# Performance work log

Measured on AMD Instinct MI355X. Metric: run time of the kernel, lower is better.

## Reference

```python
import math
import jax, jax.numpy as jnp
import numpy as np

# static config (mirrors init_kwargs / input_specs)
B, HRV, WRV, CRV = 2, 32, 1024, 64
CB, HB, WB = 256, 200, 200
D, COUT, HEADS, POINTS = 128, 128, 8, 6
DH = D // HEADS
RMAX = 55.0
XMIN, XMAX, YMIN, YMAX = -50.0, 50.0, -50.0, 50.0


def group_norm(x, gamma, beta, groups, eps=1e-5):
    b, h, w, c = x.shape
    xg = x.reshape(b, h, w, groups, c // groups)
    mean = xg.mean(axis=(1, 2, 4), keepdims=True)
    var = xg.var(axis=(1, 2, 4), keepdims=True)
    xg = (xg - mean) * jax.lax.rsqrt(var + eps)
    return xg.reshape(b, h, w, c) * gamma + beta


def fwd(x_rv, bev, pq_w, pq_b, pv_w, pv_b, po_w, po_b, qs_w1, qs_b1, qs_w2, qs_b2,
        rh_w1, rh_b1, rh_g1, rh_be1, rh_w2, rh_g2, rh_be2, rh_w3, rh_b3,
        so_w, so_b, aw_w, aw_b, vp_w, vp_b, op_w, op_b):
    b = x_rv.shape[0]
    nq = HRV * WRV
    az = jnp.linspace(-math.pi, math.pi, WRV + 1)[:-1]  # [Wrv]
    az = jnp.broadcast_to(az[None, None, :], (b, HRV, WRV))
    coord = jnp.stack([jnp.sin(az), jnp.cos(az), jnp.zeros_like(az)], axis=-1)  # [b,H,W,3]
    Q0 = x_rv @ pq_w + pq_b                                  # 1x1 conv as matmul (NHWC)
    Vmap = bev.transpose(0, 2, 3, 1) @ pv_w + pv_b           # [b,HB,WB,D]
    # range head: 1x1 conv -> GN(8) -> GELU -> 3x3 circular conv -> GN(8) -> GELU -> 1x1 conv
    h = jnp.concatenate([x_rv, coord], axis=-1) @ rh_w1 + rh_b1
    h = jax.nn.gelu(group_norm(h, rh_g1, rh_be1, 8), approximate=False)
    hp = jnp.pad(h, ((0, 0), (1, 1), (1, 1), (0, 0)), mode='wrap')  # circular padding
    h = jax.lax.conv_general_dilated(hp, rh_w2, (1, 1), 'VALID',
                                     dimension_numbers=('NHWC', 'HWIO', 'NHWC'))
    h = jax.nn.gelu(group_norm(h, rh_g2, rh_be2, 8), approximate=False)
    rh = h @ rh_w3 + rh_b3                                   # [b,H,W,2]
    mu = jnp.clip(rh[..., 0], 0.0, RMAX)                     # [b,H,W]
    log_sigma = jnp.clip(rh[..., 1:2], -5.0, 3.0)            # [b,H,W,1]
    sigma = jnp.exp(log_sigma)
    x_mu = mu * jnp.cos(az)
    y_mu = mu * jnp.sin(az)
    rx = jnp.clip((x_mu - XMIN) / (XMAX - XMIN), 0.0, 1.0)
    ry = jnp.clip((y_mu - YMIN) / (YMAX - YMIN), 0.0, 1.0)
    ref = jnp.stack([rx, ry], axis=-1).reshape(b, nq, 2)
    sig_feat = jnp.concatenate([log_sigma, 1.0 / (sigma + 1e-6)], axis=-1)
    q = jnp.concatenate([Q0, sig_feat], axis=-1) @ qs_w1 + qs_b1
    q = jax.nn.gelu(q, approximate=False) @ qs_w2 + qs_b2
    query = q.reshape(b, nq, D)
    # ---- MSDA (num_levels = 1) ----
    value = Vmap.reshape(b, HB * WB, D) @ vp_w + vp_b
    vflat = value.reshape(b, HB * WB, HEADS, DH).transpose(0, 2, 1, 3)  # [b,heads,NV,dh]
    offs = (query @ so_w + so_b).reshape(b, nq, HEADS, POINTS, 2)
    attw = jax.nn.softmax((query @ aw_w + aw_b).reshape(b, nq, HEADS, POINTS), axis=-1)
    norm = jnp.array([WB, HB], dtype=query.dtype)            # offset_normalizer = [W, H]
    loc = ref[:, :, None, None, :] + offs / norm             # [b,nq,heads,P,2] in [0,1]
    loc = loc.transpose(0, 2, 1, 3, 4)                       # [b,heads,nq,P,2]
    attw = attw.transpose(0, 2, 1, 3)                        # [b,heads,nq,P]
    # grid_sample bilinear, zero padding, align_corners=False: pix = loc*size - 0.5
    px = loc[..., 0] * WB - 0.5
    py = loc[..., 1] * HB - 0.5
    x0 = jnp.floor(px).astype(jnp.int32)
    y0 = jnp.floor(py).astype(jnp.int32)
    wx = px - x0
    wy = py - y0

    def gather(xi, yi):
        valid = (xi >= 0) & (xi < WB) & (yi >= 0) & (yi < HB)
        idx = jnp.clip(yi, 0, HB - 1) * WB + jnp.clip(xi, 0, WB - 1)
        g = jnp.take_along_axis(vflat, idx.reshape(b, HEADS, nq * POINTS, 1), axis=2)
        return g.reshape(b, HEADS, nq, POINTS, DH) * valid[..., None]

    sampled = (gather(x0, y0) * ((1 - wx) * (1 - wy))[..., None]
               + gather(x0 + 1, y0) * (wx * (1 - wy))[..., None]
               + gather(x0, y0 + 1) * ((1 - wx) * wy)[..., None]
               + gather(x0 + 1, y0 + 1) * (wx * wy)[..., None])    # [b,heads,nq,P,dh]
    out = (sampled * attw[..., None]).sum(axis=3)                  # [b,heads,nq,dh]
    out = out.transpose(0, 2, 1, 3).reshape(b, nq, D) @ op_w + op_b
    y = out.reshape(b, HRV, WRV, D) @ po_w + po_b                  # proj_o (1x1 conv)
    return y                                                       # [b,Hrv,Wrv,C_out]


def setup_inputs() -> dict:
    key = jax.random.key(0)
    ks = jax.random.split(key, 20)
    def rn(i, shape, s=0.02):
        return s * jax.random.normal(ks[i], shape, jnp.float32)
    z = lambda n: jnp.zeros((n,), jnp.float32)
    o = lambda n: jnp.ones((n,), jnp.float32)
    return dict(
        x_rv=rn(0, (B, HRV, WRV, CRV), 1.0),
        bev=rn(1, (B, CB, HB, WB), 1.0),
        pq_w=rn(2, (CRV, D)), pq_b=z(D),
        pv_w=rn(3, (CB, D)), pv_b=z(D),
        po_w=rn(4, (D, COUT)), po_b=z(COUT),
        qs_w1=rn(5, (D + 2, D)), qs_b1=z(D),
        qs_w2=rn(6, (D, D)), qs_b2=z(D),
        rh_w1=rn(7, (CRV + 3, 128)), rh_b1=z(128),
        rh_g1=o(128), rh_be1=z(128),
        rh_w2=rn(8, (3, 3, 128, 64)),
        rh_g2=o(64), rh_be2=z(64),
        rh_w3=rn(9, (64, 2)), rh_b3=z(2),
        so_w=rn(10, (D, HEADS * POINTS * 2)), so_b=rn(11, (HEADS * POINTS * 2,), 0.5),
        aw_w=rn(12, (D, HEADS * POINTS)), aw_b=z(HEADS * POINTS),
        vp_w=rn(13, (D, D)), vp_b=z(D),
        op_w=rn(14, (D, D)), op_b=z(D),
    )


def reference(x_rv, bev, pq_w, pq_b, pv_w, pv_b, po_w, po_b, qs_w1, qs_b1, qs_w2, qs_b2,
              rh_w1, rh_b1, rh_g1, rh_be1, rh_w2, rh_g2, rh_be2, rh_w3, rh_b3,
              so_w, so_b, aw_w, aw_b, vp_w, vp_b, op_w, op_b):
    return fwd(x_rv, bev, pq_w, pq_b, pv_w, pv_b, po_w, po_b, qs_w1, qs_b1, qs_w2, qs_b2,
               rh_w1, rh_b1, rh_g1, rh_be1, rh_w2, rh_g2, rh_be2, rh_w3, rh_b3,
               so_w, so_b, aw_w, aw_b, vp_w, vp_b, op_w, op_b)
```

## Files before the change

kernel.cpp:

```cpp
#include <hip/hip_runtime.h>
#include <math.h>

#define PI_F 3.14159265358979323846f


typedef __attribute__((ext_vector_type(8))) short bf16x8;
typedef __attribute__((ext_vector_type(4))) float f32x4;

__device__ __forceinline__ float gelu_f(float x) {
    return 0.5f * x * (1.0f + erff(x * 0.70710678118654752440f));
}

__device__ __forceinline__ unsigned short f2bf(float x) {
    unsigned int u = __float_as_uint(x);
    u += 0x7fffu + ((u >> 16) & 1u);
    return (unsigned short)(u >> 16);
}

__device__ __forceinline__ float bf2f(unsigned short h) {
    return __uint_as_float((unsigned int)h << 16);
}

__global__ void prep_weights(const float* __restrict__ pv_w, const float* __restrict__ pv_b,
                             const float* __restrict__ vp_w, const float* __restrict__ vp_b,
                             const float* __restrict__ op_w, const float* __restrict__ op_b,
                             const float* __restrict__ po_w, const float* __restrict__ po_b,
                             const float* __restrict__ pq_w, const float* __restrict__ pq_b,
                             const float* __restrict__ qs_w1, const float* __restrict__ qs_b1,
                             const float* __restrict__ qs_w2, const float* __restrict__ qs_b2,
                             const float* __restrict__ so_w, const float* __restrict__ so_b,
                             const float* __restrict__ aw_w, const float* __restrict__ aw_b,
                             const float* __restrict__ rh_w2,
                             unsigned short* __restrict__ wvh, unsigned short* __restrict__ wvl,
                             float* __restrict__ pvvp_b,
                             float* __restrict__ oppo_w, float* __restrict__ oppo_b,
                             float* __restrict__ pqqs_w, float* __restrict__ pqqs_b,
                             float* __restrict__ qsso_w, float* __restrict__ qsso_b,
                             float* __restrict__ qsaw_w, float* __restrict__ qsaw_b,
                             unsigned short* __restrict__ wtb,
                             float2* __restrict__ azsc) {
    int r = blockIdx.x;
    int d = threadIdx.x;
    if (r < 256) {
        float s = 0.f;
        for (int k = 0; k < 128; ++k) s += pv_w[r * 128 + k] * vp_w[k * 128 + d];
        unsigned short h = f2bf(s);
        int dt = d >> 4, mm = d & 15;
        int kc = r >> 5, qd = (r >> 3) & 3, jj = r & 7;
        size_t off = (((size_t)(dt * 8 + kc) * 64) + qd * 16 + mm) * 8 + jj;
        wvh[off] = h;
        wvl[off] = f2bf(s - bf2f(h));
    } else if (r == 256) {
        float s = vp_b[d];
        for (int k = 0; k < 128; ++k) s += pv_b[k] * vp_w[k * 128 + d];
        pvvp_b[d] = s;
    } else if (r < 385) {
        int rr = r - 257;
        float s = 0.f;
        for (int k = 0; k < 128; ++k) s += op_w[rr * 128 + k] * po_w[k * 128 + d];
        oppo_w[rr * 128 + d] = s;
    } else if (r == 385) {
        float s = po_b[d];
        for (int k = 0; k < 128; ++k) s += op_b[k] * po_w[k * 128 + d];
        oppo_b[d] = s;
    } else if (r < 450) {
        int rr = r - 386;
        float s = 0.f;
        for (int k = 0; k < 128; ++k) s += pq_w[rr * 128 + k] * qs_w1[k * 128 + d];
        pqqs_w[rr * 128 + d] = s;
    } else if (r == 450) {
        float s = qs_b1[d];
        for (int k = 0; k < 128; ++k) s += pq_b[k] * qs_w1[k * 128 + d];
        pqqs_b[d] = s;
    } else if (r < 459) {
        int w = (r - 451) * 128 + d;
        float az = -PI_F + (float)w * (6.283185307179586f / 1024.0f);
        azsc[w] = make_float2(sinf(az), cosf(az));
    } else if (r < 587) {
        int rr = r - 459;
        if (d < 96) {
            float s = 0.f;
            for (int k = 0; k < 128; ++k) s += qs_w2[rr * 128 + k] * so_w[k * 96 + d];
            qsso_w[rr * 96 + d] = s;
        }
    } else if (r == 587) {
        if (d < 96) {
            float s = so_b[d];
            for (int k = 0; k < 128; ++k) s += qs_b2[k] * so_w[k * 96 + d];
            qsso_b[d] = s;
        }
    } else if (r < 716) {
        int rr = r - 588;
        if (d < 48) {
            float s = 0.f;
            for (int k = 0; k < 128; ++k) s += qs_w2[rr * 128 + k] * aw_w[k * 48 + d];
            qsaw_w[rr * 48 + d] = s;
        }
    } else if (r == 716) {
        if (d < 48) {
            float s = aw_b[d];
            for (int k = 0; k < 128; ++k) s += qs_b2[k] * aw_w[k * 48 + d];
            qsaw_b[d] = s;
        }
    } else {
        int idx = (r - 717) * 128 + d;
        int ci = idx & 31;
        int o = (idx >> 5) & 63;
        int cc4i = (idx >> 11) & 3;
        int tap = idx >> 13;
        float w = rh_w2[((size_t)tap * 128 + cc4i * 32 + ci) * 64 + o];
        wtb[idx] = f2bf(w);
    }
}

template <int NT, bool STATS>
__global__ __launch_bounds__(2 * NT) void gemm_v3(
    const float* __restrict__ A, int lda,
    const float* __restrict__ W,
    const float* __restrict__ bias,
    float* __restrict__ C, int K,
    const float2* __restrict__ azsc,
    const float* __restrict__ extra2,
    const float* __restrict__ extra_w,
    int emode, int do_gelu, float* __restrict__ stats1) {
    constexpr int NTH = 2 * NT;
    constexpr int NTO = NT / 8;
    __shared__ float As[32][140];
    __shared__ float Ws[32][NT];
    __shared__ float sred[8][2];
    const int tid = threadIdx.x;
    const int tn = tid % NTO;
    const int tm = tid / NTO;
    const int m0 = blockIdx.x * 128;
    if (STATS && tid < 16) sred[tid >> 1][tid & 1] = 0.f;
    float acc[8][8];
#pragma unroll
    for (int i = 0; i < 8; ++i)
#pragma unroll
        for (int j = 0; j < 8; ++j) acc[i][j] = 0.f;

    for (int k0 = 0; k0 < K; k0 += 32) {
        __syncthreads();
        for (int f = tid; f < 1024; f += NTH) {
            int r = f >> 3, c4 = f & 7;
            float4 v = *(const float4*)(A + (size_t)(m0 + r) * lda + k0 + c4 * 4);
            As[c4 * 4 + 0][r] = v.x;
            As[c4 * 4 + 1][r] = v.y;
            As[c4 * 4 + 2][r] = v.z;
            As[c4 * 4 + 3][r] = v.w;
        }
        for (int f = tid; f < 8 * NT; f += NTH) {
            int kk = f / (NT / 4), n4 = f % (NT / 4);
            *(float4*)&Ws[kk][n4 * 4] = *(const float4*)(W + (size_t)(k0 + kk) * NT + n4 * 4);
        }
        __syncthreads();
#pragma unroll 2
        for (int k = 0; k < 32; ++k) {
            const float4 a0 = *(const float4*)&As[k][tm * 8];
            const float4 a1 = *(const float4*)&As[k][tm * 8 + 4];
            const float4 w0 = *(const float4*)&Ws[k][tn * 8];
            const float4 w1 = *(const float4*)&Ws[k][tn * 8 + 4];
            const float av[8] = {a0.x, a0.y, a0.z, a0.w, a1.x, a1.y, a1.z, a1.w};
            const float wv[8] = {w0.x, w0.y, w0.z, w0.w, w1.x, w1.y, w1.z, w1.w};
#pragma unroll
            for (int i = 0; i < 8; ++i)
#pragma unroll
                for (int j = 0; j < 8; ++j) acc[i][j] += av[i] * wv[j];
        }
    }
    float bv[8], e0w[8], e1w[8];
#pragma unroll
    for (int j = 0; j < 8; ++j) bv[j] = bias[tn * 8 + j];
    if (emode) {
#pragma unroll
        for (int j = 0; j < 8; ++j) {
            e0w[j] = extra_w[tn * 8 + j];
            e1w[j] = extra_w[NT + tn * 8 + j];
        }
    }
    float ts = 0.f, ts2 = 0.f;
#pragma unroll
    for (int i = 0; i < 8; ++i) {
        int m = m0 + tm * 8 + i;
        float e0 = 0.f, e1 = 0.f;
        if (emode == 1) {
            float2 sc = azsc[m & 1023];
            e0 = sc.x; e1 = sc.y;
        } else if (emode == 2) {
            e0 = extra2[2 * (size_t)m];
            e1 = extra2[2 * (size_t)m + 1];
        }
        float o[8];
#pragma unroll
        for (int j = 0; j < 8; ++j) {
            float v = acc[i][j] + bv[j];
            if (emode) v += e0 * e0w[j] + e1 * e1w[j];
            if (do_gelu) v = gelu_f(v);
            if (STATS) { ts += v; ts2 += v * v; }
            o[j] = v;
        }
        *(float4*)(C + (size_t)m * NT + tn * 8) = make_float4(o[0], o[1], o[2], o[3]);
        *(float4*)(C + (size_t)m * NT + tn * 8 + 4) = make_float4(o[4], o[5], o[6], o[7]);
    }
    if (STATS) {
        atomicAdd(&sred[tn >> 1][0], ts);
        atomicAdd(&sred[tn >> 1][1], ts2);
        __syncthreads();
        if (tid < 8) {
            int b = m0 >> 15;
            atomicAdd(&stats1[(b * 8 + tid) * 2 + 0], sred[tid][0]);
            atomicAdd(&stats1[(b * 8 + tid) * 2 + 1], sred[tid][1]);
        }
    }
}

template <int MT, int NT, int NTH>
__global__ __launch_bounds__(NTH) void gemm_rn(
    const float* __restrict__ A, int lda,
    const float* __restrict__ W, int ldw,
    const float* __restrict__ bias,
    float* __restrict__ C, int ldc, int K) {
    static_assert(NTH == (MT / 8) * (NT / 4), "thread count mismatch");
    __shared__ float As[32][MT + 12];
    __shared__ float Ws[32][NT];
    constexpr int NTN = NT / 4;
    const int tid = threadIdx.x;
    const int tn = tid % NTN;
    const int tm = tid / NTN;
    const int m0 = blockIdx.x * MT;
    float acc[8][4];
#pragma unroll
    for (int i = 0; i < 8; ++i)
#pragma unroll
        for (int j = 0; j < 4; ++j) acc[i][j] = 0.f;

    for (int k0 = 0; k0 < K; k0 += 32) {
        __syncthreads();
        for (int f = tid; f < MT * 8; f += NTH) {
            int r = f >> 3, c4 = f & 7;
            float4 v = *(const float4*)(A + (size_t)(m0 + r) * lda + k0 + c4 * 4);
            As[c4 * 4 + 0][r] = v.x;
            As[c4 * 4 + 1][r] = v.y;
            As[c4 * 4 + 2][r] = v.z;
            As[c4 * 4 + 3][r] = v.w;
        }
        for (int f = tid; f < 8 * NT; f += NTH) {
            int kk = f / NTN, n4 = f % NTN;
            *(float4*)&Ws[kk][n4 * 4] = *(const float4*)(W + (size_t)(k0 + kk) * ldw + n4 * 4);
        }
        __syncthreads();
#pragma unroll 4
        for (int k = 0; k < 32; ++k) {
            const float4 a0 = *(const float4*)&As[k][tm * 8];
            const float4 a1 = *(const float4*)&As[k][tm * 8 + 4];
            const float4 wv = *(const float4*)&Ws[k][tn * 4];
            acc[0][0] += a0.x * wv.x; acc[0][1] += a0.x * wv.y; acc[0][2] += a0.x * wv.z; acc[0][3] += a0.x * wv.w;
            acc[1][0] += a0.y * wv.x; acc[1][1] += a0.y * wv.y; acc[1][2] += a0.y * wv.z; acc[1][3] += a0.y * wv.w;
            acc[2][0] += a0.z * wv.x; acc[2][1] += a0.z * wv.y; acc[2][2] += a0.z * wv.z; acc[2][3] += a0.z * wv.w;
            acc[3][0] += a0.w * wv.x; acc[3][1] += a0.w * wv.y; acc[3][2] += a0.w * wv.z; acc[3][3] += a0.w * wv.w;
            acc[4][0] += a1.x * wv.x; acc[4][1] += a1.x * wv.y; acc[4][2] += a1.x * wv.z; acc[4][3] += a1.x * wv.w;
            acc[5][0] += a1.y * wv.x; acc[5][1] += a1.y * wv.y; acc[5][2] += a1.y * wv.z; acc[5][3] += a1.y * wv.w;
            acc[6][0] += a1.z * wv.x; acc[6][1] += a1.z * wv.y; acc[6][2] += a1.z * wv.z; acc[6][3] += a1.z * wv.w;
            acc[7][0] += a1.w * wv.x; acc[7][1] += a1.w * wv.y; acc[7][2] += a1.w * wv.z; acc[7][3] += a1.w * wv.w;
        }
    }
#pragma unroll
    for (int i = 0; i < 8; ++i) {
        int m = m0 + tm * 8 + i;
        float4 o;
        o.x = acc[i][0] + bias[tn * 4 + 0];
        o.y = acc[i][1] + bias[tn * 4 + 1];
        o.z = acc[i][2] + bias[tn * 4 + 2];
        o.w = acc[i][3] + bias[tn * 4 + 3];
        *(float4*)(C + (size_t)m * ldc + tn * 4) = o;
    }
}

__global__ __launch_bounds__(256) void value_gemm_fused(
    const float* __restrict__ bev,
    const unsigned short* __restrict__ Wh, const unsigned short* __restrict__ Wl,
    const float* __restrict__ bf, float* __restrict__ V) {
    __shared__ __align__(16) float T0[32 * 70];
    __shared__ __align__(16) float T1[32 * 70];
    const int tid = threadIdx.x;
    const int wid = tid >> 6;
    const int lane = tid & 63;
    const int m = lane & 15;
    const int quad = lane >> 4;
    const int n0 = blockIdx.x * 64;
    const int b = blockIdx.y;
    const int wn = wid >> 1;
    const int wd = wid & 1;
    const float* src = bev + (size_t)b * 256 * 40000;

    int srow[2], scol[2];
    const float* sp[2];
#pragma unroll
    for (int i = 0; i < 2; ++i) {
        int f = tid + i * 256;
        srow[i] = f >> 4;
        scol[i] = (f & 15) * 4;
        sp[i] = src + n0 + scol[i];
    }

    f32x4 acc[2][4];
#pragma unroll
    for (int i = 0; i < 2; ++i)
#pragma unroll
        for (int j = 0; j < 4; ++j) acc[i][j] = (f32x4){0.f, 0.f, 0.f, 0.f};

    const int dt0 = wd * 4;
    size_t bb[4];
#pragma unroll
    for (int j = 0; j < 4; ++j) bb[j] = (size_t)(dt0 + j) * 4096 + lane * 8;

    union UV { uint4 u; bf16x8 v; };
    float4 st[2];

#define LOADG(K0)                                                           \
    {                                                                       \
        _Pragma("unroll")                                                   \
        for (int i_ = 0; i_ < 2; ++i_)                                      \
            st[i_] = *(const float4*)(sp[i_] + (size_t)((K0) + srow[i_]) * 40000); \
    }
#define WRITELDS(TB)                                                        \
    {                                                                       \
        _Pragma("unroll")                                                   \
        for (int i_ = 0; i_ < 2; ++i_) {                                    \
            float* d_ = (TB) + srow[i_] * 70 + scol[i_];                    \
            *(float2*)(d_ + 0) = make_float2(st[i_].x, st[i_].y);           \
            *(float2*)(d_ + 2) = make_float2(st[i_].z, st[i_].w);           \
        }                                                                   \
    }

    float* Tc = T0;
    float* Tn = T1;
    LOADG(0);
    WRITELDS(Tc);
    LOADG(32);
    asm volatile("s_waitcnt lgkmcnt(0)" ::: "memory");
    __builtin_amdgcn_sched_barrier(0);
    __builtin_amdgcn_s_barrier();
    __builtin_amdgcn_sched_barrier(0);

    for (int t = 0; t < 8; ++t) {
        bf16x8 ah[2], al[2];
#pragma unroll
        for (int i = 0; i < 2; ++i) {
            const int nc = wn * 32 + i * 16 + m;
            float f8[8];
#pragma unroll
            for (int jj = 0; jj < 8; ++jj)
                f8[jj] = Tc[(quad * 8 + jj) * 70 + nc];
            unsigned hh[4], ll[4];
#pragma unroll
            for (int q = 0; q < 4; ++q) {
                unsigned u0 = __float_as_uint(f8[2 * q]);
                unsigned u1 = __float_as_uint(f8[2 * q + 1]);
                hh[q] = __builtin_amdgcn_perm(u1, u0, 0x07060302);
                float l0 = f8[2 * q] - __uint_as_float(u0 & 0xffff0000u);
                float l1 = f8[2 * q + 1] - __uint_as_float(u1 & 0xffff0000u);
                asm("v_cvt_pk_bf16_f32 %0, %1, %2" : "=v"(ll[q]) : "v"(l0), "v"(l1));
            }
            UV th, tl;
            th.u = make_uint4(hh[0], hh[1], hh[2], hh[3]);
            tl.u = make_uint4(ll[0], ll[1], ll[2], ll[3]);
            ah[i] = th.v;
            al[i] = tl.v;
        }
        if (t < 7) WRITELDS(Tn);
        if (t < 6) LOADG(t * 32 + 64);
        bf16x8 bh[4], bl[4];
#pragma unroll
        for (int j = 0; j < 4; ++j) {
            bh[j] = *(const bf16x8*)(Wh + bb[j] + t * 512);
            bl[j] = *(const bf16x8*)(Wl + bb[j] + t * 512);
        }
#pragma unroll
        for (int i = 0; i < 2; ++i)
#pragma unroll
            for (int j = 0; j < 4; ++j) {
                acc[i][j] = __builtin_amdgcn_mfma_f32_16x16x32_bf16(ah[i], bh[j], acc[i][j], 0, 0, 0);
                acc[i][j] = __builtin_amdgcn_mfma_f32_16x16x32_bf16(ah[i], bl[j], acc[i][j], 0, 0, 0);
                acc[i][j] = __builtin_amdgcn_mfma_f32_16x16x32_bf16(al[i], bh[j], acc[i][j], 0, 0, 0);
            }
        if (t < 7) {
            asm volatile("s_waitcnt lgkmcnt(0)" ::: "memory");
            __builtin_amdgcn_sched_barrier(0);
            __builtin_amdgcn_s_barrier();
            __builtin_amdgcn_sched_barrier(0);
            float* tmp = Tc; Tc = Tn; Tn = tmp;
        }
    }
#undef LOADG
#undef WRITELDS
    float bv[4];
#pragma unroll
    for (int j = 0; j < 4; ++j) bv[j] = bf[wd * 64 + j * 16 + m];
#pragma unroll
    for (int i = 0; i < 2; ++i) {
        int nbase = n0 + wn * 32 + i * 16 + quad * 4;
#pragma unroll
        for (int r = 0; r < 4; ++r) {
            int n = nbase + r;
            float* vp = V + ((size_t)b * 40000 + n) * 128 + wd * 64 + m;
#pragma unroll
            for (int j = 0; j < 4; ++j) vp[j * 16] = acc[i][j][r] + bv[j];
        }
    }
}

__global__ __launch_bounds__(256) void gn1_bf16(
    const float* __restrict__ X, const float* __restrict__ stats,
    const float* __restrict__ g1, const float* __restrict__ be1,
    unsigned short* __restrict__ Ob) {
    size_t i4 = (size_t)blockIdx.x * 256 + threadIdx.x;
    size_t base = i4 * 4;
    int c = (int)(base & 127);
    int mrow = (int)(base >> 7);
    int b = mrow >> 15;
    int g = c >> 4;
    float mean = stats[(b * 8 + g) * 2 + 0] * (1.0f / 524288.0f);
    float var = stats[(b * 8 + g) * 2 + 1] * (1.0f / 524288.0f) - mean * mean;
    float rs = 1.0f / sqrtf(var + 1e-5f);
    float4 x = *(const float4*)(X + base);
    float4 gm = *(const float4*)(g1 + c);
    float4 bt = *(const float4*)(be1 + c);
    ushort4 o;
    o.x = f2bf(gelu_f((x.x - mean) * rs * gm.x + bt.x));
    o.y = f2bf(gelu_f((x.y - mean) * rs * gm.y + bt.y));
    o.z = f2bf(gelu_f((x.z - mean) * rs * gm.z + bt.z));
    o.w = f2bf(gelu_f((x.w - mean) * rs * gm.w + bt.w));
    *(ushort4*)(Ob + base) = o;
}

__global__ __launch_bounds__(256, 4) void conv3x3_mfma(
    const unsigned short* __restrict__ H1b,
    const unsigned short* __restrict__ Wtb,
    float* __restrict__ Y,
    float* __restrict__ stats2) {
    __shared__ short As_s[66 * 40];
    __shared__ short Ws_s[3 * 64 * 40];
    __shared__ float sred[8][2];
    const int tid = threadIdx.x;
    const int wid = tid >> 6;
    const int lane = tid & 63;
    const int m = lane & 15;
    const int quad = lane >> 4;
    const int x0 = blockIdx.x * 64;
    const int y = blockIdx.y;
    const int b = blockIdx.z;
    if (tid < 16) sred[tid >> 1][tid & 1] = 0.f;
    f32x4 acc[4];
#pragma unroll
    for (int oq = 0; oq < 4; ++oq) acc[oq] = (f32x4){0.f, 0.f, 0.f, 0.f};

    const unsigned short* Hb = H1b + (size_t)b * 32 * 1024 * 128;
    for (int ry = 0; ry < 3; ++ry) {
        const int gy = (y + ry + 31) & 31;
        const unsigned short* Hrow = Hb + (size_t)gy * 1024 * 128;
        for (int cc4 = 0; cc4 < 4; ++cc4) {
            __syncthreads();
            for (int f = tid; f < 264; f += 256) {
                int xx = f >> 2, cq = f & 3;
                int gx = (x0 + xx + 1023) & 1023;
                uint4 v = *(const uint4*)(Hrow + (size_t)gx * 128 + cc4 * 32 + cq * 8);
                *(uint4*)&As_s[xx * 40 + cq * 8] = v;
            }
            for (int f = tid; f < 768; f += 256) {
                int cq = f & 3, o = (f >> 2) & 63, dx = f >> 8;
                int tap = ry * 3 + dx;
                uint4 v = *(const uint4*)(Wtb + ((size_t)(tap * 4 + cc4) * 64 + o) * 32 + cq * 8);
                *(uint4*)&Ws_s[(dx * 64 + o) * 40 + cq * 8] = v;
            }
            __syncthreads();
            const int arow = wid * 16 + m;
#pragma unroll
            for (int dx = 0; dx < 3; ++dx) {
                bf16x8 a = *(const bf16x8*)&As_s[(arow + dx) * 40 + quad * 8];
#pragma unroll
                for (int oq = 0; oq < 4; ++oq) {
                    bf16x8 bfr = *(const bf16x8*)&Ws_s[(dx * 64 + oq * 16 + m) * 40 + quad * 8];
                    acc[oq] = __builtin_amdgcn_mfma_f32_16x16x32_bf16(a, bfr, acc[oq], 0, 0, 0);
                }
            }
        }
    }
    float sv[4], qv[4];
#pragma unroll
    for (int oq = 0; oq < 4; ++oq) {
        sv[oq] = acc[oq].x + acc[oq].y + acc[oq].z + acc[oq].w;
        qv[oq] = acc[oq].x * acc[oq].x + acc[oq].y * acc[oq].y +
                 acc[oq].z * acc[oq].z + acc[oq].w * acc[oq].w;
    }
    const int masks[5] = {1, 2, 4, 16, 32};
#pragma unroll
    for (int mi = 0; mi < 5; ++mi) {
#pragma unroll
        for (int oq = 0; oq < 4; ++oq) {
            sv[oq] += __shfl_xor(sv[oq], masks[mi]);
            qv[oq] += __shfl_xor(qv[oq], masks[mi]);
        }
    }
    if ((lane & 55) == 0) {
        int gb = (lane >> 3) & 1;
#pragma unroll
        for (int oq = 0; oq < 4; ++oq) {
            atomicAdd(&sred[oq * 2 + gb][0], sv[oq]);
            atomicAdd(&sred[oq * 2 + gb][1], qv[oq]);
        }
    }
    const int pxb = x0 + wid * 16 + quad * 4;
    float* Yb = Y + ((size_t)(b * 32 + y) * 1024 + pxb) * 64;
#pragma unroll
    for (int oq = 0; oq < 4; ++oq) {
        const float av[4] = {acc[oq].x, acc[oq].y, acc[oq].z, acc[oq].w};
#pragma unroll
        for (int r = 0; r < 4; ++r) Yb[(size_t)r * 64 + oq * 16 + m] = av[r];
    }
    __syncthreads();
    if (tid < 16)
        atomicAdd(&stats2[(b * 8 + (tid >> 1)) * 2 + (tid & 1)], sred[tid >> 1][tid & 1]);
}

__global__ __launch_bounds__(256) void rh3_kernel(
    const float* __restrict__ H2, const float* __restrict__ stats,
    const float* __restrict__ gamma, const float* __restrict__ beta, float inv_cnt,
    const float* __restrict__ w3, const float* __restrict__ b3,
    const float2* __restrict__ azsc,
    float2* __restrict__ refxy, float2* __restrict__ sigf) {
    const int tid = threadIdx.x;
    const int lane = tid & 15;
    const int m = blockIdx.x * 16 + (tid >> 4);
    const int b = m >> 15;
    const int c = lane * 4;
    const int g = c >> 3;
    float mean = stats[(b * 8 + g) * 2 + 0] * inv_cnt;
    float var = stats[(b * 8 + g) * 2 + 1] * inv_cnt - mean * mean;
    float rs = 1.0f / sqrtf(var + 1e-5f);
    float4 v = *(const float4*)(H2 + (size_t)m * 64 + c);
    float hv[4];
    hv[0] = gelu_f((v.x - mean) * rs * gamma[c + 0] + beta[c + 0]);
    hv[1] = gelu_f((v.y - mean) * rs * gamma[c + 1] + beta[c + 1]);
    hv[2] = gelu_f((v.z - mean) * rs * gamma[c + 2] + beta[c + 2]);
    hv[3] = gelu_f((v.w - mean) * rs * gamma[c + 3] + beta[c + 3]);
    float d0 = 0.f, d1 = 0.f;
#pragma unroll
    for (int k = 0; k < 4; ++k) {
        d0 += hv[k] * w3[(c + k) * 2 + 0];
        d1 += hv[k] * w3[(c + k) * 2 + 1];
    }
#pragma unroll
    for (int s = 1; s < 16; s <<= 1) {
        d0 += __shfl_xor(d0, s, 16);
        d1 += __shfl_xor(d1, s, 16);
    }
    if (lane == 0) {
        float mu = fminf(fmaxf(d0 + b3[0], 0.f), 55.f);
        float ls = fminf(fmaxf(d1 + b3[1], -5.f), 3.f);
        float sg = expf(ls);
        float2 sc = azsc[m & 1023];
        float rx = fminf(fmaxf(mu * sc.y * 0.01f + 0.5f, 0.f), 1.f);
        float ry = fminf(fmaxf(mu * sc.x * 0.01f + 0.5f, 0.f), 1.f);
        refxy[m] = make_float2(rx, ry);
        sigf[m] = make_float2(ls, 1.f / (sg + 1e-6f));
    }
}

__global__ __launch_bounds__(256) void msda_kernel(
    const float* __restrict__ V, const float2* __restrict__ refxy,
    const float* __restrict__ offs, const float* __restrict__ aw,
    float* __restrict__ out) {
    const int tid = threadIdx.x;
    const int l4 = tid & 3;
    const int grp = tid >> 2;
    const int m = blockIdx.x * 8 + (grp >> 3);
    const int head = grp & 7;
    const int b = m >> 15;
    float2 r = refxy[m];
    const float* lg = aw + (size_t)m * 48 + head * 6;
    float l[6];
#pragma unroll
    for (int p = 0; p < 6; ++p) l[p] = lg[p];
    float mx = l[0];
#pragma unroll
    for (int p = 1; p < 6; ++p) mx = fmaxf(mx, l[p]);
    float s = 0.f;
#pragma unroll
    for (int p = 0; p < 6; ++p) { l[p] = expf(l[p] - mx); s += l[p]; }
    float inv = 1.f / s;
#pragma unroll
    for (int p = 0; p < 6; ++p) l[p] *= inv;
    const float* of = offs + (size_t)m * 96 + head * 12;
    const float* Vb = V + (size_t)b * 40000 * 128 + head * 16 + l4 * 4;
    const float bx = r.x * 200.f - 0.5f;
    const float by = r.y * 200.f - 0.5f;
    f32x4 acc = (f32x4){0.f, 0.f, 0.f, 0.f};
#pragma unroll
    for (int p = 0; p < 6; ++p) {
        float px = bx + of[p * 2 + 0];
        float py = by + of[p * 2 + 1];
        float fx = floorf(px), fy = floorf(py);
        int x0 = (int)fx, y0 = (int)fy;
        float wx = px - fx, wy = py - fy;
        int xc0 = min(max(x0, 0), 199), xc1 = min(max(x0 + 1, 0), 199);
        int yc0 = min(max(y0, 0), 199), yc1 = min(max(y0 + 1, 0), 199);
        bool vx0 = ((unsigned)x0 < 200u), vx1 = ((unsigned)(x0 + 1) < 200u);
        bool vy0 = ((unsigned)y0 < 200u), vy1 = ((unsigned)(y0 + 1) < 200u);
        const f32x4 v00 = *(const f32x4*)(Vb + ((size_t)(yc0 * 200 + xc0)) * 128);
        const f32x4 v10 = *(const f32x4*)(Vb + ((size_t)(yc0 * 200 + xc1)) * 128);
        const f32x4 v01 = *(const f32x4*)(Vb + ((size_t)(yc1 * 200 + xc0)) * 128);
        const f32x4 v11 = *(const f32x4*)(Vb + ((size_t)(yc1 * 200 + xc1)) * 128);
        float w = l[p];
        float w00 = (vx0 && vy0) ? w * (1.f - wx) * (1.f - wy) : 0.f;
        float w10 = (vx1 && vy0) ? w * wx * (1.f - wy) : 0.f;
        float w01 = (vx0 && vy1) ? w * (1.f - wx) * wy : 0.f;
        float w11 = (vx1 && vy1) ? w * wx * wy : 0.f;
        acc += v00 * w00;
        acc += v10 * w10;
        acc += v01 * w01;
        acc += v11 * w11;
    }
    *(f32x4*)(out + (size_t)m * 128 + head * 16 + l4 * 4) = acc;
}

extern "C" void kernel_launch(void* const* d_in, const int* in_sizes, int n_in,
                              void* d_out, int out_size, void* d_ws, size_t ws_size,
                              hipStream_t stream) {
    const float* x_rv = (const float*)d_in[0];
    const float* bev = (const float*)d_in[1];
    const float* pq_w = (const float*)d_in[2];
    const float* pq_b = (const float*)d_in[3];
    const float* pv_w = (const float*)d_in[4];
    const float* pv_b = (const float*)d_in[5];
    const float* po_w = (const float*)d_in[6];
    const float* po_b = (const float*)d_in[7];
    const float* qs_w1 = (const float*)d_in[8];
    const float* qs_b1 = (const float*)d_in[9];
    const float* qs_w2 = (const float*)d_in[10];
    const float* qs_b2 = (const float*)d_in[11];
    const float* rh_w1 = (const float*)d_in[12];
    const float* rh_b1 = (const float*)d_in[13];
    const float* rh_g1 = (const float*)d_in[14];
    const float* rh_be1 = (const float*)d_in[15];
    const float* rh_w2 = (const float*)d_in[16];
    const float* rh_g2 = (const float*)d_in[17];
    const float* rh_be2 = (const float*)d_in[18];
    const float* rh_w3 = (const float*)d_in[19];
    const float* rh_b3 = (const float*)d_in[20];
    const float* so_w = (const float*)d_in[21];
    const float* so_b = (const float*)d_in[22];
    const float* aw_w = (const float*)d_in[23];
    const float* aw_b = (const float*)d_in[24];
    const float* vp_w = (const float*)d_in[25];
    const float* vp_b = (const float*)d_in[26];
    const float* op_w = (const float*)d_in[27];
    const float* op_b = (const float*)d_in[28];

    const int M = 65536;

    float* ws = (float*)d_ws;
    float* azsc = ws;    ws += 2048;
    unsigned short* wvh = (unsigned short*)ws; ws += 16384;
    unsigned short* wvl = (unsigned short*)ws; ws += 16384;
    float* pvvp_b = ws;  ws += 128;
    float* oppo_w = ws;  ws += 128 * 128;
    float* oppo_b = ws;  ws += 128;
    float* pqqs_w = ws;  ws += 64 * 128;
    float* pqqs_b = ws;  ws += 128;
    float* qsso_w = ws;  ws += 128 * 96;
    float* qsso_b = ws;  ws += 128;
    float* qsaw_w = ws;  ws += 128 * 48;
    float* qsaw_b = ws;  ws += 64;
    float* stats = ws;   ws += 64;
    unsigned short* wtb = (unsigned short*)ws;  ws += 36864;
    unsigned short* h1b = (unsigned short*)ws;  ws += (size_t)M * 64;
    float* Vv = ws;      ws += (size_t)80000 * 128;
    float* h1 = ws;      ws += (size_t)M * 128;
    float* h2 = ws;      ws += (size_t)M * 64;
    float* q1 = ws;      ws += (size_t)M * 128;
    float* refxy = ws;   ws += (size_t)M * 2;
    float* sigf = ws;    ws += (size_t)M * 2;
    size_t need_bytes = (size_t)(ws - (float*)d_ws) * sizeof(float);
    if (ws_size < need_bytes) return;
    float* offs = h1;
    float* attw = h2;
    float* mo = q1;

    float2* azsc2 = (float2*)azsc;
    float2* refxy2 = (float2*)refxy;
    float2* sigf2 = (float2*)sigf;

    prep_weights<<<1293, 128, 0, stream>>>(
        pv_w, pv_b, vp_w, vp_b, op_w, op_b, po_w, po_b, pq_w, pq_b,
        qs_w1, qs_b1, qs_w2, qs_b2, so_w, so_b, aw_w, aw_b, rh_w2,
        wvh, wvl, pvvp_b, oppo_w, oppo_b, pqqs_w, pqqs_b,
        qsso_w, qsso_b, qsaw_w, qsaw_b, wtb, azsc2);
    hipMemsetAsync(stats, 0, 64 * sizeof(float), stream);

    value_gemm_fused<<<dim3(625, 2), 256, 0, stream>>>(bev, wvh, wvl, pvvp_b, Vv);

    gemm_v3<128, true><<<M / 128, 256, 0, stream>>>(
        x_rv, 64, rh_w1, rh_b1, h1, 64, azsc2, nullptr, rh_w1 + 64 * 128, 1, 0, stats);

    gn1_bf16<<<8192, 256, 0, stream>>>(h1, stats, rh_g1, rh_be1, h1b);

    conv3x3_mfma<<<dim3(16, 32, 2), 256, 0, stream>>>(h1b, wtb, h2, stats + 32);

    rh3_kernel<<<4096, 256, 0, stream>>>(h2, stats + 32, rh_g2, rh_be2, 1.0f / 262144.0f,
                                         rh_w3, rh_b3, azsc2, refxy2, sigf2);

    gemm_v3<128, false><<<M / 128, 256, 0, stream>>>(
        x_rv, 64, pqqs_w, pqqs_b, q1, 64, nullptr, sigf, qs_w1 + 128 * 128, 2, 1, nullptr);

    gemm_v3<96, false><<<M / 128, 192, 0, stream>>>(
        q1, 128, qsso_w, qsso_b, offs, 128, nullptr, nullptr, nullptr, 0, 0, nullptr);

    gemm_rn<128, 48, 192><<<M / 128, 192, 0, stream>>>(
        q1, 128, qsaw_w, 48, qsaw_b, attw, 48, 128);

    msda_kernel<<<M / 8, 256, 0, stream>>>(Vv, refxy2, offs, attw, mo);

    gemm_v3<128, false><<<M / 128, 256, 0, stream>>>(
        mo, 128, oppo_w, oppo_b, (float*)d_out, 128, nullptr, nullptr, nullptr, 0, 0, nullptr);
}
```

Baseline: 464.4 us.

## Move query, offset/attention and output GEMMs to split-bf16 MFMA kernel

Replaces the fp32 SIMT GEMMs for the query projection, sampling-offset, attention-weight and output projections with a generic MFMA kernel. It uses 3-pass hi/lo bf16 splitting to keep near-fp32 accuracy. Weights are pre-packed into MFMA fragment layout in prep_weights. The offset and attention-weight GEMMs are fused into one launch over a concatenated weight matrix, so q1 is read once. This trades three MFMA passes and in-kernel A splitting for matrix-core throughput, and the GELU/bias/sigma epilogue is folded in.

```diff
diff --git a/kernel.cpp b/kernel.cpp
--- a/kernel.cpp
+++ b/kernel.cpp
@@ -19,6 +19,11 @@
 
 __device__ __forceinline__ float bf2f(unsigned short h) {
     return __uint_as_float((unsigned int)h << 16);
+}
+
+__device__ __forceinline__ size_t fragoff(int k, int c, int KC, int tilebase) {
+    return (((size_t)((tilebase + (c >> 4)) * KC + (k >> 5)) * 64) +
+            ((k >> 3) & 3) * 16 + (c & 15)) * 8 + (k & 7);
 }
 
 __global__ void prep_weights(const float* __restrict__ pv_w, const float* __restrict__ pv_b,
@@ -33,10 +38,12 @@
                              const float* __restrict__ rh_w2,
                              unsigned short* __restrict__ wvh, unsigned short* __restrict__ wvl,
                              float* __restrict__ pvvp_b,
-                             float* __restrict__ oppo_w, float* __restrict__ oppo_b,
-                             float* __restrict__ pqqs_w, float* __restrict__ pqqs_b,
-                             float* __restrict__ qsso_w, float* __restrict__ qsso_b,
-                             float* __restrict__ qsaw_w, float* __restrict__ qsaw_b,
+                             unsigned short* __restrict__ woh, unsigned short* __restrict__ wol,
+                             float* __restrict__ oppo_b,
+                             unsigned short* __restrict__ wqh, unsigned short* __restrict__ wql,
+                             float* __restrict__ pqqs_b,
+                             unsigned short* __restrict__ wah, unsigned short* __restrict__ wal,
+                             float* __restrict__ qab,
                              unsigned short* __restrict__ wtb,
                              float2* __restrict__ azsc) {
     int r = blockIdx.x;
@@ -45,9 +52,7 @@
         float s = 0.f;
         for (int k = 0; k < 128; ++k) s += pv_w[r * 128 + k] * vp_w[k * 128 + d];
         unsigned short h = f2bf(s);
-        int dt = d >> 4, mm = d & 15;
-        int kc = r >> 5, qd = (r >> 3) & 3, jj = r & 7;
-        size_t off = (((size_t)(dt * 8 + kc) * 64) + qd * 16 + mm) * 8 + jj;
+        size_t off = fragoff(r, d, 8, 0);
         wvh[off] = h;
         wvl[off] = f2bf(s - bf2f(h));
     } else if (r == 256) {
@@ -58,7 +63,10 @@
         int rr = r - 257;
         float s = 0.f;
         for (int k = 0; k < 128; ++k) s += op_w[rr * 128 + k] * po_w[k * 128 + d];
-        oppo_w[rr * 128 + d] = s;
+        unsigned short h = f2bf(s);
+        size_t off = fragoff(rr, d, 4, 0);
+        woh[off] = h;
+        wol[off] = f2bf(s - bf2f(h));
     } else if (r == 385) {
         float s = po_b[d];
         for (int k = 0; k < 128; ++k) s += op_b[k] * po_w[k * 128 + d];
@@ -67,7 +75,10 @@
         int rr = r - 386;
         float s = 0.f;
         for (int k = 0; k < 128; ++k) s += pq_w[rr * 128 + k] * qs_w1[k * 128 + d];
-        pqqs_w[rr * 128 + d] = s;
+        unsigned short h = f2bf(s);
+        size_t off = fragoff(rr, d, 2, 0);
+        wqh[off] = h;
+        wql[off] = f2bf(s - bf2f(h));
     } else if (r == 450) {
         float s = qs_b1[d];
         for (int k = 0; k < 128; ++k) s += pq_b[k] * qs_w1[k * 128 + d];
@@ -81,26 +92,32 @@
         if (d < 96) {
             float s = 0.f;
             for (int k = 0; k < 128; ++k) s += qs_w2[rr * 128 + k] * so_w[k * 96 + d];
-            qsso_w[rr * 96 + d] = s;
+            unsigned short h = f2bf(s);
+            size_t off = fragoff(rr, d, 4, 0);
+            wah[off] = h;
+            wal[off] = f2bf(s - bf2f(h));
         }
     } else if (r == 587) {
         if (d < 96) {
             float s = so_b[d];
             for (int k = 0; k < 128; ++k) s += qs_b2[k] * so_w[k * 96 + d];
-            qsso_b[d] = s;
+            qab[d] = s;
         }
     } else if (r < 716) {
         int rr = r - 588;
         if (d < 48) {
             float s = 0.f;
             for (int k = 0; k < 128; ++k) s += qs_w2[rr * 128 + k] * aw_w[k * 48 + d];
-            qsaw_w[rr * 48 + d] = s;
+            unsigned short h = f2bf(s);
+            size_t off = fragoff(rr, d, 4, 6);
+            wah[off] = h;
+            wal[off] = f2bf(s - bf2f(h));
         }
     } else if (r == 716) {
         if (d < 48) {
             float s = aw_b[d];
             for (int k = 0; k < 128; ++k) s += qs_b2[k] * aw_w[k * 48 + d];
-            qsaw_b[d] = s;
+            qab[96 + d] = s;
         }
     } else {
         int idx = (r - 717) * 128 + d;
@@ -214,65 +231,147 @@
     }
 }
 
-template <int MT, int NT, int NTH>
-__global__ __launch_bounds__(NTH) void gemm_rn(
-    const float* __restrict__ A, int lda,
-    const float* __restrict__ W, int ldw,
+template <int KC, int NJ, int EMODE, int GELU, int DUAL>
+__global__ __launch_bounds__(256) void gemm_mf(
+    const float* __restrict__ A,
+    const unsigned short* __restrict__ Bh, const unsigned short* __restrict__ Bl,
     const float* __restrict__ bias,
-    float* __restrict__ C, int ldc, int K) {
-    static_assert(NTH == (MT / 8) * (NT / 4), "thread count mismatch");
-    __shared__ float As[32][MT + 12];
-    __shared__ float Ws[32][NT];
-    constexpr int NTN = NT / 4;
+    float* __restrict__ C1, float* __restrict__ C2,
+    const float2* __restrict__ ex2, const float* __restrict__ exw) {
+    constexpr int K = KC * 32;
+    __shared__ __align__(16) float T0[32 * 70];
+    __shared__ __align__(16) float T1[32 * 70];
     const int tid = threadIdx.x;
-    const int tn = tid % NTN;
-    const int tm = tid / NTN;
-    const int m0 = blockIdx.x * MT;
-    float acc[8][4];
-#pragma unroll
-    for (int i = 0; i < 8; ++i)
-#pragma unroll
-        for (int j = 0; j < 4; ++j) acc[i][j] = 0.f;
-
-    for (int k0 = 0; k0 < K; k0 += 32) {
-        __syncthreads();
-        for (int f = tid; f < MT * 8; f += NTH) {
-            int r = f >> 3, c4 = f & 7;
-            float4 v = *(const float4*)(A + (size_t)(m0 + r) * lda + k0 + c4 * 4);
-            As[c4 * 4 + 0][r] = v.x;
-            As[c4 * 4 + 1][r] = v.y;
-            As[c4 * 4 + 2][r] = v.z;
-            As[c4 * 4 + 3][r] = v.w;
-        }
-        for (int f = tid; f < 8 * NT; f += NTH) {
-            int kk = f / NTN, n4 = f % NTN;
-            *(float4*)&Ws[kk][n4 * 4] = *(const float4*)(W + (size_t)(k0 + kk) * ldw + n4 * 4);
-        }
-        __syncthreads();
-#pragma unroll 4
-        for (int k = 0; k < 32; ++k) {
-            const float4 a0 = *(const float4*)&As[k][tm * 8];
-            const float4 a1 = *(const float4*)&As[k][tm * 8 + 4];
-            const float4 wv = *(const float4*)&Ws[k][tn * 4];
-            acc[0][0] += a0.x * wv.x; acc[0][1] += a0.x * wv.y; acc[0][2] += a0.x * wv.z; acc[0][3] += a0.x * wv.w;
-            acc[1][0] += a0.y * wv.x; acc[1][1] += a0.y * wv.y; acc[1][2] += a0.y * wv.z; acc[1][3] += a0.y * wv.w;
-            acc[2][0] += a0.z * wv.x; acc[2][1] += a0.z * wv.y; acc[2][2] += a0.z * wv.z; acc[2][3] += a0.z * wv.w;
-            acc[3][0] += a0.w * wv.x; acc[3][1] += a0.w * wv.y; acc[3][2] += a0.w * wv.z; acc[3][3] += a0.w * wv.w;
-            acc[4][0] += a1.x * wv.x; acc[4][1] += a1.x * wv.y; acc[4][2] += a1.x * wv.z; acc[4][3] += a1.x * wv.w;
-            acc[5][0] += a1.y * wv.x; acc[5][1] += a1.y * wv.y; acc[5][2] += a1.y * wv.z; acc[5][3] += a1.y * wv.w;
-            acc[6][0] += a1.z * wv.x; acc[6][1] += a1.z * wv.y; acc[6][2] += a1.z * wv.z; acc[6][3] += a1.z * wv.w;
-            acc[7][0] += a1.w * wv.x; acc[7][1] += a1.w * wv.y; acc[7][2] += a1.w * wv.z; acc[7][3] += a1.w * wv.w;
-        }
-    }
-#pragma unroll
-    for (int i = 0; i < 8; ++i) {
-        int m = m0 + tm * 8 + i;
-        float4 o;
-        o.x = acc[i][0] + bias[tn * 4 + 0];
-        o.y = acc[i][1] + bias[tn * 4 + 1];
-        o.z = acc[i][2] + bias[tn * 4 + 2];
-        o.w = acc[i][3] + bias[tn * 4 + 3];
-        *(float4*)(C + (size_t)m * ldc + tn * 4) = o;
+    const int wid = tid >> 6;
+    const int lane = tid & 63;
+    const int mm = lane & 15;
+    const int quad = lane >> 4;
+    const int m0 = blockIdx.x * 64;
+
+    int srow[2], scol[2];
+    const float* sp[2];
+#pragma unroll
+    for (int i = 0; i < 2; ++i) {
+        int f = tid + i * 256;
+        srow[i] = f >> 3;
+        scol[i] = (f & 7) * 4;
+        sp[i] = A + (size_t)(m0 + srow[i]) * K + scol[i];
+    }
+
+    f32x4 acc[NJ];
+#pragma unroll
+    for (int j = 0; j < NJ; ++j) acc[j] = (f32x4){0.f, 0.f, 0.f, 0.f};
+
+    union UV { uint4 u; bf16x8 v; };
+    float4 st[2];
+
+#define LOADG(K0)                                                 \
+    {                                                             \
+        _Pragma("unroll")                                         \
+        for (int i_ = 0; i_ < 2; ++i_)                            \
+            st[i_] = *(const float4*)(sp[i_] + (K0));             \
+    }
+#define WRITELDS(TB)                                              \
+    {                                                             \
+        _Pragma("unroll")                                         \
+        for (int i_ = 0; i_ < 2; ++i_) {                          \
+            _Pragma("unroll")                                     \
+            for (int c_ = 0; c_ < 4; ++c_)                        \
+                (TB)[(scol[i_] + c_) * 70 + srow[i_]] = st[i_][c_]; \
+        }                                                         \
+    }
+#define BARRIER()                                                 \
+    asm volatile("s_waitcnt lgkmcnt(0)" ::: "memory");            \
+    __builtin_amdgcn_sched_barrier(0);                            \
+    __builtin_amdgcn_s_barrier();                                 \
+    __builtin_amdgcn_sched_barrier(0);
+
+    float* Tc = T0;
+    float* Tn = T1;
+    LOADG(0);
+    WRITELDS(Tc);
+    if (KC > 1) LOADG(32);
+    BARRIER();
+
+#pragma unroll
+    for (int t = 0; t < KC; ++t) {
+        bf16x8 ah, al;
+        {
+            const int nc = wid * 16 + mm;
+            float f8[8];
+#pragma unroll
+            for (int jj = 0; jj < 8; ++jj)
+                f8[jj] = Tc[(quad * 8 + jj) * 70 + nc];
+            unsigned hh[4], ll[4];
+#pragma unroll
+            for (int q = 0; q < 4; ++q) {
+                unsigned u0 = __float_as_uint(f8[2 * q]);
+                unsigned u1 = __float_as_uint(f8[2 * q + 1]);
+                hh[q] = __builtin_amdgcn_perm(u1, u0, 0x07060302);
+                float l0 = f8[2 * q] - __uint_as_float(u0 & 0xffff0000u);
+                float l1 = f8[2 * q + 1] - __uint_as_float(u1 & 0xffff0000u);
+                asm("v_cvt_pk_bf16_f32 %0, %1, %2" : "=v"(ll[q]) : "v"(l0), "v"(l1));
+            }
+            UV th, tl;
+            th.u = make_uint4(hh[0], hh[1], hh[2], hh[3]);
+            tl.u = make_uint4(ll[0], ll[1], ll[2], ll[3]);
+            ah = th.v;
+            al = tl.v;
+        }
+        if (t < KC - 1) WRITELDS(Tn);
+        if (t < KC - 2) LOADG((t + 2) * 32);
+        bf16x8 bh[NJ], bl[NJ];
+#pragma unroll
+        for (int j = 0; j < NJ; ++j) {
+            size_t o = ((size_t)(j * KC + t) * 64 + lane) * 8;
+            bh[j] = *(const bf16x8*)(Bh + o);
+            bl[j] = *(const bf16x8*)(Bl + o);
+        }
+#pragma unroll
+        for (int j = 0; j < NJ; ++j) {
+            acc[j] = __builtin_amdgcn_mfma_f32_16x16x32_bf16(ah, bh[j], acc[j], 0, 0, 0);
+            acc[j] = __builtin_amdgcn_mfma_f32_16x16x32_bf16(ah, bl[j], acc[j], 0, 0, 0);
+            acc[j] = __builtin_amdgcn_mfma_f32_16x16x32_bf16(al, bh[j], acc[j], 0, 0, 0);
+        }
+        if (t < KC - 1) {
+            BARRIER();
+            float* tmp = Tc; Tc = Tn; Tn = tmp;
+        }
+    }
+#undef LOADG
+#undef WRITELDS
+#undef BARRIER
+    float bvj[NJ];
+#pragma unroll
+    for (int j = 0; j < NJ; ++j) bvj[j] = bias[j * 16 + mm];
+    float2 ev[4];
+    float e0w[NJ], e1w[NJ];
+    if (EMODE) {
+#pragma unroll
+        for (int r = 0; r < 4; ++r) ev[r] = ex2[m0 + wid * 16 + quad * 4 + r];
+#pragma unroll
+        for (int j = 0; j < NJ; ++j) {
+            e0w[j] = exw[j * 16 + mm];
+            e1w[j] = exw[128 + j * 16 + mm];
+        }
+    }
+#pragma unroll
+    for (int j = 0; j < NJ; ++j) {
+        float* Cp;
+        int col, ldc;
+        if (DUAL && j >= 6) {
+            Cp = C2; col = (j - 6) * 16 + mm; ldc = 48;
+        } else {
+            Cp = C1; col = j * 16 + mm; ldc = DUAL ? 96 : NJ * 16;
+        }
+#pragma unroll
+        for (int r = 0; r < 4; ++r) {
+            int row = m0 + wid * 16 + quad * 4 + r;
+            float v = acc[j][r] + bvj[j];
+            if (EMODE) v += ev[r].x * e0w[j] + ev[r].y * e1w[j];
+            if (GELU) v = gelu_f(v);
+            Cp[(size_t)row * ldc + col] = v;
+        }
     }
 }
 
@@ -664,14 +763,15 @@
     unsigned short* wvh = (unsigned short*)ws; ws += 16384;
     unsigned short* wvl = (unsigned short*)ws; ws += 16384;
     float* pvvp_b = ws;  ws += 128;
-    float* oppo_w = ws;  ws += 128 * 128;
+    unsigned short* woh = (unsigned short*)ws; ws += 8192;
+    unsigned short* wol = (unsigned short*)ws; ws += 8192;
     float* oppo_b = ws;  ws += 128;
-    float* pqqs_w = ws;  ws += 64 * 128;
+    unsigned short* wqh = (unsigned short*)ws; ws += 4096;
+    unsigned short* wql = (unsigned short*)ws; ws += 4096;
     float* pqqs_b = ws;  ws += 128;
-    float* qsso_w = ws;  ws += 128 * 96;
-    float* qsso_b = ws;  ws += 128;
-    float* qsaw_w = ws;  ws += 128 * 48;
-    float* qsaw_b = ws;  ws += 64;
+    unsigned short* wah = (unsigned short*)ws; ws += 9216;
+    unsigned short* wal = (unsigned short*)ws; ws += 9216;
+    float* qab = ws;     ws += 144;
     float* stats = ws;   ws += 64;
     unsigned short* wtb = (unsigned short*)ws;  ws += 36864;
     unsigned short* h1b = (unsigned short*)ws;  ws += (size_t)M * 64;
@@ -694,8 +794,8 @@
     prep_weights<<<1293, 128, 0, stream>>>(
         pv_w, pv_b, vp_w, vp_b, op_w, op_b, po_w, po_b, pq_w, pq_b,
         qs_w1, qs_b1, qs_w2, qs_b2, so_w, so_b, aw_w, aw_b, rh_w2,
-        wvh, wvl, pvvp_b, oppo_w, oppo_b, pqqs_w, pqqs_b,
-        qsso_w, qsso_b, qsaw_w, qsaw_b, wtb, azsc2);
+        wvh, wvl, pvvp_b, woh, wol, oppo_b, wqh, wql, pqqs_b,
+        wah, wal, qab, wtb, azsc2);
     hipMemsetAsync(stats, 0, 64 * sizeof(float), stream);
 
     value_gemm_fused<<<dim3(625, 2), 256, 0, stream>>>(bev, wvh, wvl, pvvp_b, Vv);
@@ -710,17 +810,14 @@
     rh3_kernel<<<4096, 256, 0, stream>>>(h2, stats + 32, rh_g2, rh_be2, 1.0f / 262144.0f,
                                          rh_w3, rh_b3, azsc2, refxy2, sigf2);
 
-    gemm_v3<128, false><<<M / 128, 256, 0, stream>>>(
-        x_rv, 64, pqqs_w, pqqs_b, q1, 64, nullptr, sigf, qs_w1 + 128 * 128, 2, 1, nullptr);
-
-    gemm_v3<96, false><<<M / 128, 192, 0, stream>>>(
-        q1, 128, qsso_w, qsso_b, offs, 128, nullptr, nullptr, nullptr, 0, 0, nullptr);
-
-    gemm_rn<128, 48, 192><<<M / 128, 192, 0, stream>>>(
-        q1, 128, qsaw_w, 48, qsaw_b, attw, 48, 128);
+    gemm_mf<2, 8, 1, 1, 0><<<M / 64, 256, 0, stream>>>(
+        x_rv, wqh, wql, pqqs_b, q1, nullptr, sigf2, qs_w1 + 128 * 128);
+
+    gemm_mf<4, 9, 0, 0, 1><<<M / 64, 256, 0, stream>>>(
+        q1, wah, wal, qab, offs, attw, nullptr, nullptr);
 
     msda_kernel<<<M / 8, 256, 0, stream>>>(Vv, refxy2, offs, attw, mo);
 
-    gemm_v3<128, false><<<M / 128, 256, 0, stream>>>(
-        mo, 128, oppo_w, oppo_b, (float*)d_out, 128, nullptr, nullptr, nullptr, 0, 0, nullptr);
-}
+    gemm_mf<4, 8, 0, 0, 0><<<M / 64, 256, 0, stream>>>(
+        mo, woh, wol, oppo_b, (float*)d_out, nullptr, nullptr, nullptr);
+}
```

Measured after the change: 397.1 us. 1.17x faster.
